# Optimization experiments

Measured on AMD Instinct MI355X. Metric: run time of the kernel, lower is better.

Reference implementation:

```python
import jax, jax.numpy as jnp
import numpy as np

N, E, D, NHID, NOUT, G = 50000, 800000, 128, 512, 768, 512
EPS = 1e-5

def setup_inputs() -> dict:
    key = jax.random.key(0)
    ks = jax.random.split(key, 20)
    rn = lambda k, s: jax.random.normal(k, s, jnp.float32) * 0.05
    inp = {
        'x': jax.random.normal(ks[0], (N, D), jnp.float32),
        'edge_index': jax.random.randint(ks[1], (2, E), 0, N, jnp.int32),
        'batch': jnp.sort(jax.random.randint(ks[2], (N,), 0, G, jnp.int32)),
        # GCN convs 1..3 (weights stored [in, out])
        'W1': rn(ks[3], (D, D)), 'b1': jnp.zeros((D,), jnp.float32),
        'W2': rn(ks[4], (D, D)), 'b2': jnp.zeros((D,), jnp.float32),
        'W3': rn(ks[5], (D, D)), 'b3': jnp.zeros((D,), jnp.float32),
        # GAT attention layer (1 head)
        'Wa': rn(ks[6], (D, D)), 'ba': jnp.zeros((D,), jnp.float32),
        'a_src': rn(ks[7], (D,)), 'a_dst': rn(ks[8], (D,)),
        # BatchNorms: bn1, bn2, bn3, bn_attention stacked [4, D]
        'bn_gamma': jnp.ones((4, D), jnp.float32),
        'bn_beta': jnp.zeros((4, D), jnp.float32),
        # MLP head
        'Wm1': rn(ks[9], (D, NHID)), 'bm1': jnp.zeros((NHID,), jnp.float32),
        'Wm2': rn(ks[10], (NHID, NHID)), 'bm2': jnp.zeros((NHID,), jnp.float32),
        'Wm3': rn(ks[11], (NHID, NHID)), 'bm3': jnp.zeros((NHID,), jnp.float32),
        'Wm4': rn(ks[12], (NHID, NOUT)), 'bm4': jnp.zeros((NOUT,), jnp.float32),
    }
    return inp

def _bn(h, g, b):
    # BatchNorm1d over nodes, training-mode batch stats (biased variance)
    m = jnp.mean(h, axis=0)
    v = jnp.var(h, axis=0)
    return (h - m) * jax.lax.rsqrt(v + EPS) * g + b

def _gcn(x, W, b, src, dst, deg_isqrt):
    h = x @ W                               # [N, D]
    norm = deg_isqrt[src] * deg_isqrt[dst]  # [E+N]
    msg = h[src] * norm[:, None]            # gather + scale
    return jax.ops.segment_sum(msg, dst, num_segments=N) + b

def _gat(x, W, b, a_src, a_dst, src, dst):
    h = x @ W
    e = jax.nn.leaky_relu((h @ a_src)[src] + (h @ a_dst)[dst], 0.2)  # [E+N]
    m = jax.ops.segment_max(e, dst, num_segments=N)
    ex = jnp.exp(e - m[dst])
    den = jax.ops.segment_sum(ex, dst, num_segments=N)
    alpha = ex / den[dst]
    out = jax.ops.segment_sum(alpha[:, None] * h[src], dst, num_segments=N)
    return out + b

def reference(x, edge_index, batch, W1, b1, W2, b2, W3, b3, Wa, ba, a_src, a_dst,
              bn_gamma, bn_beta, Wm1, bm1, Wm2, bm2, Wm3, bm3, Wm4, bm4):
    # add self-loops (PyG GCNConv / GATConv default)
    loops = jnp.arange(N, dtype=edge_index.dtype)
    src = jnp.concatenate([edge_index[0], loops])
    dst = jnp.concatenate([edge_index[1], loops])
    deg = jax.ops.segment_sum(jnp.ones_like(dst, jnp.float32), dst, num_segments=N)
    deg_isqrt = jax.lax.rsqrt(deg)  # deg >= 1 thanks to self-loops

    relu = jax.nn.relu
    x = relu(_bn(_gcn(x, W1, b1, src, dst, deg_isqrt), bn_gamma[0], bn_beta[0])) + x
    x = relu(_bn(_gcn(x, W2, b2, src, dst, deg_isqrt), bn_gamma[1], bn_beta[1])) + x
    x = relu(_bn(_gcn(x, W3, b3, src, dst, deg_isqrt), bn_gamma[2], bn_beta[2])) + x
    x = relu(_bn(_gat(x, Wa, ba, a_src, a_dst, src, dst), bn_gamma[3], bn_beta[3])) + x

    # global mean pool over graphs
    counts = jax.ops.segment_sum(jnp.ones((N,), jnp.float32), batch, num_segments=G)
    pooled = jax.ops.segment_sum(x, batch, num_segments=G) / jnp.maximum(counts, 1.0)[:, None]

    h = relu(pooled @ Wm1 + bm1)
    h = relu(h @ Wm2 + bm2)
    h = relu(h @ Wm3 + bm3)
    return h @ Wm4 + bm4
```

## Files before the change

kernel.cpp:

```cpp
#include <hip/hip_runtime.h>
#include <stdint.h>

#define Nn   50000
#define Ee   800000
#define Dd   128
#define Gg   512
#define NHIDc 512
#define NOUTc 768
#define EPSf 1e-5f
#define CAP  64
#define PRNG 6250
#define NBPART 12500
#define NB2    250

#define OFF_CNT    0ul
#define OFF_ES     200192ul
#define OFF_ED     400384ul
#define OFF_STATS  600576ul
#define OFF_POOLED 601600ul
#define OFF_M1     863744ul
#define OFF_M2     1912320ul
#define OFF_COL    2960896ul
#define OFF_H      15760896ul
#define OFF_AGG    28560896ul
#define OFF_XCUR   41360896ul
#define OFF_PART   54160896ul
#define OFF_XBF    66960896ul

#define BF_LO(u) __uint_as_float((u) << 16)
#define BF_HI(u) __uint_as_float((u) & 0xffff0000u)

typedef __attribute__((ext_vector_type(8))) short bf16x8;
typedef __attribute__((ext_vector_type(4))) float f32x4;

__device__ inline uint32_t bfpack(float x, float y) {
    uint32_t ux = __float_as_uint(x), uy = __float_as_uint(y);
    ux += 0x7fff + ((ux >> 16) & 1);
    uy += 0x7fff + ((uy >> 16) & 1);
    return (ux >> 16) | (uy & 0xffff0000u);
}
__device__ inline short bf1(float x) {
    uint32_t u = __float_as_uint(x);
    u += 0x7fff + ((u >> 16) & 1);
    return (short)(u >> 16);
}
__device__ inline float wred16(float v) {
    v += __shfl_xor(v, 1); v += __shfl_xor(v, 2);
    v += __shfl_xor(v, 4); v += __shfl_xor(v, 8);
    return v;
}

__global__ void k_x2bf(const float* __restrict__ x, uint32_t* __restrict__ xbf) {
    int i = blockIdx.x * 256 + threadIdx.x;
    if (i < Nn * 16) {
        float4 a = reinterpret_cast<const float4*>(x)[2 * i];
        float4 b = reinterpret_cast<const float4*>(x)[2 * i + 1];
        uint32_t o[4] = {bfpack(a.x, a.y), bfpack(a.z, a.w),
                         bfpack(b.x, b.y), bfpack(b.z, b.w)};
        reinterpret_cast<uint4*>(xbf)[i] = *reinterpret_cast<uint4*>(o);
    }
}

__global__ void k_fill_init(int* cnt, int* colx) {
    int i = blockIdx.x * 256 + threadIdx.x;
    if (i < Nn) {
        cnt[i] = 1;
        colx[(size_t)i * CAP] = i;
    }
}

__global__ void k_bucket_fill(const int* __restrict__ ei, int* cnt, int* colx) {
    int grp = blockIdx.x & 7;
    int e = (blockIdx.x >> 3) * 256 + threadIdx.x;
    if (e >= Ee) return;
    int d = ei[Ee + e];
    if (d / PRNG != grp) return;
    int s = ei[e];
    int pos = atomicAdd(&cnt[d], 1);
    if (pos < CAP) colx[(size_t)d * CAP + pos] = s;
}

#define WTP 136
__global__ __launch_bounds__(512) void k_gemm_fused(
        const uint32_t* __restrict__ XP, const uint32_t* __restrict__ AggP,
        const float* __restrict__ stats, const float* __restrict__ W,
        const int* __restrict__ cntP,
        uint32_t* __restrict__ Hout, uint32_t* __restrict__ XoutP,
        const float* __restrict__ a_src, const float* __restrict__ a_dst,
        float* __restrict__ esO, float* __restrict__ edO) {
    __shared__ short WT[128 * WTP];
    __shared__ short XT[8][16 * WTP];
    __shared__ float isqL[128];

    int t = threadIdx.x;
    for (int i = t; i < 128 * 128; i += 512) {
        int k = i >> 7, c = i & 127;
        WT[c * WTP + k] = bf1(W[i]);
    }
    __syncthreads();

    int wave = t >> 6, lane = t & 63;
    int arow = lane & 15, kg = lane >> 4;
    int c4 = (lane * 4) & 63;
    int prow = lane >> 4;
    float scv[8], shv[8];
    if (stats) {
        #pragma unroll
        for (int j = 0; j < 8; ++j) {
            scv[j] = stats[2 * c4 + j];
            shv[j] = stats[128 + 2 * c4 + j];
        }
    }
    float asr[8], adr[8];
    if (esO) {
        #pragma unroll
        for (int jj = 0; jj < 8; ++jj) {
            asr[jj] = a_src[(lane & 15) * 8 + jj];
            adr[jj] = a_dst[(lane & 15) * 8 + jj];
        }
    }

    for (int tile = blockIdx.x * 128; tile < Nn; tile += gridDim.x * 128) {
        int rbase = tile + wave * 16;
        if (lane < 16) {
            int rg = rbase + lane;
            isqL[wave * 16 + lane] = (cntP && rg < Nn) ? rsqrtf((float)cntP[rg]) : 1.f;
        }
        uint32_t* xtw = reinterpret_cast<uint32_t*>(XT[wave]);
        #pragma unroll
        for (int b = 0; b < 4; ++b) {
            int row = b * 4 + prow;
            int rg = rbase + row;
            uint32_t xv[4] = {0u, 0u, 0u, 0u};
            if (rg < Nn) {
                *reinterpret_cast<uint4*>(xv) =
                    *reinterpret_cast<const uint4*>(&XP[(size_t)rg * 64 + c4]);
                if (AggP) {
                    uint32_t av[4];
                    *reinterpret_cast<uint4*>(av) =
                        *reinterpret_cast<const uint4*>(&AggP[(size_t)rg * 64 + c4]);
                    #pragma unroll
                    for (int q = 0; q < 4; ++q) {
                        float n0 = fmaxf(BF_LO(av[q]) * scv[2 * q] + shv[2 * q], 0.f) + BF_LO(xv[q]);
                        float n1 = fmaxf(BF_HI(av[q]) * scv[2 * q + 1] + shv[2 * q + 1], 0.f) + BF_HI(xv[q]);
                        xv[q] = bfpack(n0, n1);
                    }
                    *reinterpret_cast<uint4*>(&XoutP[(size_t)rg * 64 + c4]) =
                        *reinterpret_cast<uint4*>(xv);
                }
            }
            *reinterpret_cast<uint4*>(&xtw[row * (WTP / 2) + c4]) = *reinterpret_cast<uint4*>(xv);
        }
        bf16x8 afr[4];
        #pragma unroll
        for (int kt = 0; kt < 4; ++kt)
            afr[kt] = *reinterpret_cast<bf16x8*>(&XT[wave][arow * WTP + kt * 32 + kg * 8]);
        float sR[4];
        #pragma unroll
        for (int rr = 0; rr < 4; ++rr) sR[rr] = isqL[wave * 16 + kg * 4 + rr];

        #pragma unroll
        for (int ct = 0; ct < 8; ++ct) {
            int c = ct * 16 + arow;
            f32x4 acc = {0.f, 0.f, 0.f, 0.f};
            #pragma unroll
            for (int kt = 0; kt < 4; ++kt) {
                bf16x8 b = *reinterpret_cast<bf16x8*>(&WT[c * WTP + kt * 32 + kg * 8]);
                acc = __builtin_amdgcn_mfma_f32_16x16x32_bf16(afr[kt], b, acc, 0, 0, 0);
            }
            #pragma unroll
            for (int rr = 0; rr < 4; ++rr)
                XT[wave][(kg * 4 + rr) * WTP + c] = bf1(acc[rr] * sR[rr]);
        }
        #pragma unroll
        for (int p = 0; p < 4; ++p) {
            int rsl = p * 4 + kg;
            int rg = rbase + rsl;
            if (rg < Nn) {
                int chunk = lane & 15;
                bf16x8 vv = *reinterpret_cast<bf16x8*>(&XT[wave][rsl * WTP + chunk * 8]);
                *reinterpret_cast<bf16x8*>(reinterpret_cast<short*>(Hout) + (size_t)rg * 128 + chunk * 8) = vv;
                if (esO) {
                    float dsum = 0.f, ddum = 0.f;
                    #pragma unroll
                    for (int jj = 0; jj < 8; ++jj) {
                        float hv = __uint_as_float(((uint32_t)(unsigned short)vv[jj]) << 16);
                        dsum += hv * asr[jj];
                        ddum += hv * adr[jj];
                    }
                    dsum = wred16(dsum); ddum = wred16(ddum);
                    if ((lane & 15) == 0) { esO[rg] = dsum; edO[rg] = ddum; }
                }
            }
        }
    }
}

__global__ __launch_bounds__(256) void k_gcn_agg(const uint32_t* __restrict__ H,
                                                 const int* __restrict__ cnt,
                                                 const int* __restrict__ colx,
                                                 uint32_t* __restrict__ aggP,
                                                 float* __restrict__ part) {
    int wave = threadIdx.x >> 6, lane = threadIdx.x & 63;
    int half = lane >> 5, fl = lane & 31;
    int nid = blockIdx.x * 4 + wave;
    const uint2* H2 = reinterpret_cast<const uint2*>(H);

    int degF = cnt[nid];
    int deg = degF > CAP ? CAP : degF;
    size_t cb = (size_t)nid * CAP;
    int m = (deg - half + 1) >> 1;
    float f0a = 0.f, f1a = 0.f, f2a = 0.f, f3a = 0.f;
    float f0b = 0.f, f1b = 0.f, f2b = 0.f, f3b = 0.f;
    float f0c = 0.f, f1c = 0.f, f2c = 0.f, f3c = 0.f;
    float f0d = 0.f, f1d = 0.f, f2d = 0.f, f3d = 0.f;
    int k = 0;
    for (; k + 3 < m; k += 4) {
        int s0 = colx[cb + half + 2 * k];
        int s1 = colx[cb + half + 2 * k + 2];
        int s2 = colx[cb + half + 2 * k + 4];
        int s3 = colx[cb + half + 2 * k + 6];
        uint2 u0 = H2[(size_t)s0 * 32 + fl];
        uint2 u1 = H2[(size_t)s1 * 32 + fl];
        uint2 u2 = H2[(size_t)s2 * 32 + fl];
        uint2 u3 = H2[(size_t)s3 * 32 + fl];
        f0a += BF_LO(u0.x); f1a += BF_HI(u0.x); f2a += BF_LO(u0.y); f3a += BF_HI(u0.y);
        f0b += BF_LO(u1.x); f1b += BF_HI(u1.x); f2b += BF_LO(u1.y); f3b += BF_HI(u1.y);
        f0c += BF_LO(u2.x); f1c += BF_HI(u2.x); f2c += BF_LO(u2.y); f3c += BF_HI(u2.y);
        f0d += BF_LO(u3.x); f1d += BF_HI(u3.x); f2d += BF_LO(u3.y); f3d += BF_HI(u3.y);
    }
    for (; k < m; ++k) {
        int s0 = colx[cb + half + 2 * k];
        uint2 u0 = H2[(size_t)s0 * 32 + fl];
        f0a += BF_LO(u0.x); f1a += BF_HI(u0.x); f2a += BF_LO(u0.y); f3a += BF_HI(u0.y);
    }
    float f0 = (f0a + f0b) + (f0c + f0d);
    float f1 = (f1a + f1b) + (f1c + f1d);
    float f2 = (f2a + f2b) + (f2c + f2d);
    float f3 = (f3a + f3b) + (f3c + f3d);
    f0 += __shfl_xor(f0, 32); f1 += __shfl_xor(f1, 32);
    f2 += __shfl_xor(f2, 32); f3 += __shfl_xor(f3, 32);

    float o0 = 0.f, o1 = 0.f, o2 = 0.f, o3 = 0.f;
    if (half == 0) {
        float wd = rsqrtf((float)degF);
        o0 = f0 * wd; o1 = f1 * wd; o2 = f2 * wd; o3 = f3 * wd;
        uint2 o;
        o.x = bfpack(o0, o1);
        o.y = bfpack(o2, o3);
        reinterpret_cast<uint2*>(aggP)[(size_t)nid * 32 + fl] = o;
    }
    __shared__ float SS[4][128];
    __shared__ float QQ[4][128];
    if (half == 0) {
        SS[wave][4 * fl + 0] = o0; QQ[wave][4 * fl + 0] = o0 * o0;
        SS[wave][4 * fl + 1] = o1; QQ[wave][4 * fl + 1] = o1 * o1;
        SS[wave][4 * fl + 2] = o2; QQ[wave][4 * fl + 2] = o2 * o2;
        SS[wave][4 * fl + 3] = o3; QQ[wave][4 * fl + 3] = o3 * o3;
    }
    __syncthreads();
    int t = threadIdx.x;
    if (t < 128) {
        part[blockIdx.x * 256 + t]       = (SS[0][t] + SS[1][t]) + (SS[2][t] + SS[3][t]);
        part[blockIdx.x * 256 + 128 + t] = (QQ[0][t] + QQ[1][t]) + (QQ[2][t] + QQ[3][t]);
    }
}

__global__ __launch_bounds__(256) void k_gat_agg(const uint32_t* __restrict__ H,
                                                 const int* __restrict__ cnt,
                                                 const int* __restrict__ colx,
                                                 const float* __restrict__ es,
                                                 const float* __restrict__ ed,
                                                 uint32_t* __restrict__ aggP,
                                                 float* __restrict__ part) {
    int wave = threadIdx.x >> 6, lane = threadIdx.x & 63;
    int half = lane >> 5, fl = lane & 31;
    int nid = blockIdx.x * 4 + wave;
    const uint2* H2 = reinterpret_cast<const uint2*>(H);

    int degF = cnt[nid];
    int deg = degF > CAP ? CAP : degF;
    size_t cb = (size_t)nid * CAP;
    float edd = ed[nid];
    int m = (deg - half + 1) >> 1;
    float f0a = 0.f, f1a = 0.f, f2a = 0.f, f3a = 0.f, dena = 0.f;
    float f0b = 0.f, f1b = 0.f, f2b = 0.f, f3b = 0.f, denb = 0.f;
    float f0c = 0.f, f1c = 0.f, f2c = 0.f, f3c = 0.f, denc = 0.f;
    float f0d = 0.f, f1d = 0.f, f2d = 0.f, f3d = 0.f, dend = 0.f;
    int k = 0;
    for (; k + 3 < m; k += 4) {
        int s0 = colx[cb + half + 2 * k];
        int s1 = colx[cb + half + 2 * k + 2];
        int s2 = colx[cb + half + 2 * k + 4];
        int s3 = colx[cb + half + 2 * k + 6];
        float e0 = es[s0] + edd, e1 = es[s1] + edd;
        float e2 = es[s2] + edd, e3 = es[s3] + edd;
        e0 = (e0 < 0.f) ? 0.2f * e0 : e0;
        e1 = (e1 < 0.f) ? 0.2f * e1 : e1;
        e2 = (e2 < 0.f) ? 0.2f * e2 : e2;
        e3 = (e3 < 0.f) ? 0.2f * e3 : e3;
        float w0 = __expf(e0), w1 = __expf(e1), w2 = __expf(e2), w3 = __expf(e3);
        uint2 u0 = H2[(size_t)s0 * 32 + fl];
        uint2 u1 = H2[(size_t)s1 * 32 + fl];
        uint2 u2 = H2[(size_t)s2 * 32 + fl];
        uint2 u3 = H2[(size_t)s3 * 32 + fl];
        f0a += w0 * BF_LO(u0.x); f1a += w0 * BF_HI(u0.x);
        f2a += w0 * BF_LO(u0.y); f3a += w0 * BF_HI(u0.y); dena += w0;
        f0b += w1 * BF_LO(u1.x); f1b += w1 * BF_HI(u1.x);
        f2b += w1 * BF_LO(u1.y); f3b += w1 * BF_HI(u1.y); denb += w1;
        f0c += w2 * BF_LO(u2.x); f1c += w2 * BF_HI(u2.x);
        f2c += w2 * BF_LO(u2.y); f3c += w2 * BF_HI(u2.y); denc += w2;
        f0d += w3 * BF_LO(u3.x); f1d += w3 * BF_HI(u3.x);
        f2d += w3 * BF_LO(u3.y); f3d += w3 * BF_HI(u3.y); dend += w3;
    }
    for (; k < m; ++k) {
        int s0 = colx[cb + half + 2 * k];
        float e0 = es[s0] + edd;
        e0 = (e0 < 0.f) ? 0.2f * e0 : e0;
        float w0 = __expf(e0);
        uint2 u0 = H2[(size_t)s0 * 32 + fl];
        f0a += w0 * BF_LO(u0.x); f1a += w0 * BF_HI(u0.x);
        f2a += w0 * BF_LO(u0.y); f3a += w0 * BF_HI(u0.y); dena += w0;
    }
    float f0 = (f0a + f0b) + (f0c + f0d);
    float f1 = (f1a + f1b) + (f1c + f1d);
    float f2 = (f2a + f2b) + (f2c + f2d);
    float f3 = (f3a + f3b) + (f3c + f3d);
    float den = (dena + denb) + (denc + dend);
    f0 += __shfl_xor(f0, 32); f1 += __shfl_xor(f1, 32);
    f2 += __shfl_xor(f2, 32); f3 += __shfl_xor(f3, 32);
    den += __shfl_xor(den, 32);

    float o0 = 0.f, o1 = 0.f, o2 = 0.f, o3 = 0.f;
    if (half == 0) {
        float inv = 1.f / den;
        o0 = f0 * inv; o1 = f1 * inv; o2 = f2 * inv; o3 = f3 * inv;
        uint2 o;
        o.x = bfpack(o0, o1);
        o.y = bfpack(o2, o3);
        reinterpret_cast<uint2*>(aggP)[(size_t)nid * 32 + fl] = o;
    }
    __shared__ float SS[4][128];
    __shared__ float QQ[4][128];
    if (half == 0) {
        SS[wave][4 * fl + 0] = o0; QQ[wave][4 * fl + 0] = o0 * o0;
        SS[wave][4 * fl + 1] = o1; QQ[wave][4 * fl + 1] = o1 * o1;
        SS[wave][4 * fl + 2] = o2; QQ[wave][4 * fl + 2] = o2 * o2;
        SS[wave][4 * fl + 3] = o3; QQ[wave][4 * fl + 3] = o3 * o3;
    }
    __syncthreads();
    int t = threadIdx.x;
    if (t < 128) {
        part[blockIdx.x * 256 + t]       = (SS[0][t] + SS[1][t]) + (SS[2][t] + SS[3][t]);
        part[blockIdx.x * 256 + 128 + t] = (QQ[0][t] + QQ[1][t]) + (QQ[2][t] + QQ[3][t]);
    }
}

__global__ __launch_bounds__(256) void k_bn_red1(const float* __restrict__ part,
                                                 float* __restrict__ part2) {
    int t = threadIdx.x;
    int r0 = blockIdx.x * 50;
    float acc = 0.f;
    #pragma unroll 5
    for (int r = r0; r < r0 + 50; ++r) acc += part[(size_t)r * 256 + t];
    part2[blockIdx.x * 256 + t] = acc;
}

__global__ __launch_bounds__(256) void k_bn_final(const float* __restrict__ part2, float* stats,
                                                  const float* __restrict__ gamma,
                                                  const float* __restrict__ beta) {
    int f = blockIdx.x;
    int t = threadIdx.x;
    float s = 0.f, q = 0.f;
    if (t < NB2) {
        s = part2[t * 256 + f];
        q = part2[t * 256 + 128 + f];
    }
    #pragma unroll
    for (int o = 32; o > 0; o >>= 1) { s += __shfl_xor(s, o); q += __shfl_xor(q, o); }
    __shared__ float rs[4], rq[4];
    if ((t & 63) == 0) { rs[t >> 6] = s; rq[t >> 6] = q; }
    __syncthreads();
    if (t == 0) {
        float S = (rs[0] + rs[1]) + (rs[2] + rs[3]);
        float Q = (rq[0] + rq[1]) + (rq[2] + rq[3]);
        const float invN = 1.f / (float)Nn;
        float mean = S * invN;
        float var = Q * invN - mean * mean;
        float scv = rsqrtf(var + EPSf) * gamma[f];
        stats[f] = scv;
        stats[128 + f] = beta[f] - mean * scv;
    }
}

__global__ __launch_bounds__(256) void k_pool(const uint32_t* __restrict__ AP,
                                              const float* __restrict__ stats,
                                              const uint32_t* __restrict__ XcP,
                                              const int* __restrict__ batch,
                                              float* __restrict__ pooled) {
    int g = blockIdx.x;
    int lo = 0, hi = Nn;
    while (lo < hi) { int mid = (lo + hi) >> 1; if (batch[mid] < g) lo = mid + 1; else hi = mid; }
    int start = lo;
    lo = start; hi = Nn;
    while (lo < hi) { int mid = (lo + hi) >> 1; if (batch[mid] < g + 1) lo = mid + 1; else hi = mid; }
    int end = lo;

    int f = threadIdx.x & 127, rg = threadIdx.x >> 7;
    float sc = stats[f], sh = stats[128 + f];
    float s = 0.f;
    for (int r = start + rg; r < end; r += 2) {
        uint32_t u = AP[(size_t)r * 64 + (f >> 1)];
        uint32_t ux = XcP[(size_t)r * 64 + (f >> 1)];
        float a  = (f & 1) ? BF_HI(u)  : BF_LO(u);
        float xv = (f & 1) ? BF_HI(ux) : BF_LO(ux);
        s += fmaxf(a * sc + sh, 0.f) + xv;
    }
    __shared__ float red[256];
    red[threadIdx.x] = s; __syncthreads();
    if (threadIdx.x < 128) {
        float tot = red[threadIdx.x] + red[threadIdx.x + 128];
        float cntg = (float)(end - start);
        pooled[g * Dd + threadIdx.x] = (cntg > 0.f) ? tot / cntg : 0.f;
    }
}

__global__ __launch_bounds__(256) void k_mlp32(const float* __restrict__ A,
                                               const float* __restrict__ B,
                                               const float* __restrict__ bias,
                                               float* __restrict__ C,
                                               int M, int K, int Nc, int do_relu) {
    __shared__ float Ast[64][36];
    __shared__ float Bs[64][68];

    int nbx = Nc >> 6;
    int by = blockIdx.x / nbx, bx = blockIdx.x - by * nbx;
    int r0 = by * 32, c0 = bx * 64;
    int t = threadIdx.x;
    int tc = t & 31, tr = t >> 5;

    float2 acc0 = {0, 0}, acc1 = {0, 0}, acc2 = {0, 0}, acc3 = {0, 0};

    int sar = t >> 3, sak = (t & 7) * 8;
    int sbk = t >> 2, sbc = (t & 3) * 16;

    for (int kc = 0; kc < K; kc += 64) {
        {
            const float* ap = A + (size_t)(r0 + sar) * K + kc + sak;
            float4 v0 = *reinterpret_cast<const float4*>(ap);
            float4 v1 = *reinterpret_cast<const float4*>(ap + 4);
            Ast[sak + 0][sar] = v0.x; Ast[sak + 1][sar] = v0.y;
            Ast[sak + 2][sar] = v0.z; Ast[sak + 3][sar] = v0.w;
            Ast[sak + 4][sar] = v1.x; Ast[sak + 5][sar] = v1.y;
            Ast[sak + 6][sar] = v1.z; Ast[sak + 7][sar] = v1.w;
        }
        {
            const float* bp = B + (size_t)(kc + sbk) * Nc + c0 + sbc;
            float4 w0 = *reinterpret_cast<const float4*>(bp);
            float4 w1 = *reinterpret_cast<const float4*>(bp + 4);
            float4 w2 = *reinterpret_cast<const float4*>(bp + 8);
            float4 w3 = *reinterpret_cast<const float4*>(bp + 12);
            *reinterpret_cast<float4*>(&Bs[sbk][sbc]) = w0;
            *reinterpret_cast<float4*>(&Bs[sbk][sbc + 4]) = w1;
            *reinterpret_cast<float4*>(&Bs[sbk][sbc + 8]) = w2;
            *reinterpret_cast<float4*>(&Bs[sbk][sbc + 12]) = w3;
        }
        __syncthreads();
        #pragma unroll 8
        for (int k = 0; k < 64; ++k) {
            float4 a = *reinterpret_cast<float4*>(&Ast[k][tr * 4]);
            float2 b = *reinterpret_cast<float2*>(&Bs[k][tc * 2]);
            acc0.x += a.x * b.x; acc0.y += a.x * b.y;
            acc1.x += a.y * b.x; acc1.y += a.y * b.y;
            acc2.x += a.z * b.x; acc2.y += a.z * b.y;
            acc3.x += a.w * b.x; acc3.y += a.w * b.y;
        }
        __syncthreads();
    }

    float b0 = bias[c0 + tc * 2], b1 = bias[c0 + tc * 2 + 1];
    float2 r[4] = {{acc0.x + b0, acc0.y + b1}, {acc1.x + b0, acc1.y + b1},
                   {acc2.x + b0, acc2.y + b1}, {acc3.x + b0, acc3.y + b1}};
    if (do_relu) {
        #pragma unroll
        for (int i = 0; i < 4; ++i) {
            r[i].x = fmaxf(r[i].x, 0.f); r[i].y = fmaxf(r[i].y, 0.f);
        }
    }
    #pragma unroll
    for (int i = 0; i < 4; ++i)
        *reinterpret_cast<float2*>(C + (size_t)(r0 + tr * 4 + i) * Nc + c0 + tc * 2) = r[i];
}

extern "C" void kernel_launch(void* const* d_in, const int* in_sizes, int n_in,
                              void* d_out, int out_size, void* d_ws, size_t ws_size,
                              hipStream_t stream) {
    const float* x       = (const float*)d_in[0];
    const int*   ei      = (const int*)d_in[1];
    const int*   batch   = (const int*)d_in[2];
    const float* W1      = (const float*)d_in[3];
    const float* W2      = (const float*)d_in[5];
    const float* W3      = (const float*)d_in[7];
    const float* Wa      = (const float*)d_in[9];
    const float* a_src   = (const float*)d_in[11];
    const float* a_dst   = (const float*)d_in[12];
    const float* bn_g    = (const float*)d_in[13];
    const float* bn_b    = (const float*)d_in[14];
    const float* Wm1     = (const float*)d_in[15];
    const float* bm1     = (const float*)d_in[16];
    const float* Wm2     = (const float*)d_in[17];
    const float* bm2     = (const float*)d_in[18];
    const float* Wm3     = (const float*)d_in[19];
    const float* bm3     = (const float*)d_in[20];
    const float* Wm4     = (const float*)d_in[21];
    const float* bm4     = (const float*)d_in[22];

    char* ws = (char*)d_ws;
    int*      cnt    = (int*)(ws + OFF_CNT);
    float*    es     = (float*)(ws + OFF_ES);
    float*    ed     = (float*)(ws + OFF_ED);
    float*    stats  = (float*)(ws + OFF_STATS);
    float*    pooled = (float*)(ws + OFF_POOLED);
    float*    m1     = (float*)(ws + OFF_M1);
    float*    m2     = (float*)(ws + OFF_M2);
    int*      colx   = (int*)(ws + OFF_COL);
    uint32_t* h      = (uint32_t*)(ws + OFF_H);
    uint32_t* aggP   = (uint32_t*)(ws + OFF_AGG);
    uint32_t* xcurP  = (uint32_t*)(ws + OFF_XCUR);
    float*    part   = (float*)(ws + OFF_PART);
    uint32_t* xbf    = (uint32_t*)(ws + OFF_XBF);
    float*    part2  = m1;

    const int nb196 = 196;
    const int nbE8  = ((Ee + 255) / 256) * 8;
    const int nbGemm = (Nn + 127) / 128;
    const int nbX2  = (Nn * 16 + 255) / 256;

    k_x2bf<<<nbX2, 256, 0, stream>>>(x, xbf);
    k_fill_init<<<nb196, 256, 0, stream>>>(cnt, colx);
    k_bucket_fill<<<nbE8, 256, 0, stream>>>(ei, cnt, colx);

    k_gemm_fused<<<nbGemm, 512, 0, stream>>>(xbf, nullptr, nullptr, W1, cnt, h, nullptr,
                                             nullptr, nullptr, nullptr, nullptr);
    k_gcn_agg<<<NBPART, 256, 0, stream>>>(h, cnt, colx, aggP, part);
    k_bn_red1<<<NB2, 256, 0, stream>>>(part, part2);
    k_bn_final<<<128, 256, 0, stream>>>(part2, stats, bn_g + 0 * Dd, bn_b + 0 * Dd);

    k_gemm_fused<<<nbGemm, 512, 0, stream>>>(xbf, aggP, stats, W2, cnt, h, xcurP,
                                             nullptr, nullptr, nullptr, nullptr);
    k_gcn_agg<<<NBPART, 256, 0, stream>>>(h, cnt, colx, aggP, part);
    k_bn_red1<<<NB2, 256, 0, stream>>>(part, part2);
    k_bn_final<<<128, 256, 0, stream>>>(part2, stats, bn_g + 1 * Dd, bn_b + 1 * Dd);

    k_gemm_fused<<<nbGemm, 512, 0, stream>>>(xcurP, aggP, stats, W3, cnt, h, xcurP,
                                             nullptr, nullptr, nullptr, nullptr);
    k_gcn_agg<<<NBPART, 256, 0, stream>>>(h, cnt, colx, aggP, part);
    k_bn_red1<<<NB2, 256, 0, stream>>>(part, part2);
    k_bn_final<<<128, 256, 0, stream>>>(part2, stats, bn_g + 2 * Dd, bn_b + 2 * Dd);

    k_gemm_fused<<<nbGemm, 512, 0, stream>>>(xcurP, aggP, stats, Wa, nullptr, h, xcurP,
                                             a_src, a_dst, es, ed);
    k_gat_agg<<<NBPART, 256, 0, stream>>>(h, cnt, colx, es, ed, aggP, part);
    k_bn_red1<<<NB2, 256, 0, stream>>>(part, part2);
    k_bn_final<<<128, 256, 0, stream>>>(part2, stats, bn_g + 3 * Dd, bn_b + 3 * Dd);

    k_pool<<<Gg, 256, 0, stream>>>(aggP, stats, xcurP, batch, pooled);

    k_mlp32<<<(Gg / 32) * (NHIDc / 64), 256, 0, stream>>>(pooled, Wm1, bm1, m1, Gg, Dd, NHIDc, 1);
    k_mlp32<<<(Gg / 32) * (NHIDc / 64), 256, 0, stream>>>(m1, Wm2, bm2, m2, Gg, NHIDc, NHIDc, 1);
    k_mlp32<<<(Gg / 32) * (NHIDc / 64), 256, 0, stream>>>(m2, Wm3, bm3, m1, Gg, NHIDc, NHIDc, 1);
    k_mlp32<<<(Gg / 32) * (NOUTc / 64), 256, 0, stream>>>(m1, Wm4, bm4, (float*)d_out, Gg, NHIDc, NOUTc, 0);
}
```

Baseline: 372.4 us.

## Merge prep kernels, fuse BN reductions with ticket, use bf16 MFMA for MLP head

Three changes. The bf16 conversion and bucket-init kernels are merged into one prep kernel. The two-stage BatchNorm statistics reduction becomes a single kernel using float atomics and a last-block ticket. The fp32 SIMT MLP head GEMMs are replaced with bf16 MFMA 16x16x32 tiles of 64x64. Together these remove several launches and speed up the small GEMMs, at the cost of bf16 rounding in the MLP and nondeterministic atomic summation order. One hazard: statsAcc and the ticket alias the m2 buffer, which the MLP head later overwrites, but the BN launches all come before that.

Measured after the change: 406.4 us. 9.1% more time.

```diff
diff --git a/kernel.cpp b/kernel.cpp
--- a/kernel.cpp
+++ b/kernel.cpp
@@ -11,7 +11,7 @@
 #define CAP  64
 #define PRNG 6250
 #define NBPART 12500
-#define NB2    250
+#define NBRED  250
 
 #define OFF_CNT    0ul
 #define OFF_ES     200192ul
@@ -50,23 +50,22 @@
     return v;
 }
 
-__global__ void k_x2bf(const float* __restrict__ x, uint32_t* __restrict__ xbf) {
+__global__ void k_prep(const float* __restrict__ x, uint32_t* __restrict__ xbf,
+                       int* cnt, int* colx, float* statsAcc, int* ticket) {
     int i = blockIdx.x * 256 + threadIdx.x;
-    if (i < Nn * 16) {
+    {
         float4 a = reinterpret_cast<const float4*>(x)[2 * i];
         float4 b = reinterpret_cast<const float4*>(x)[2 * i + 1];
         uint32_t o[4] = {bfpack(a.x, a.y), bfpack(a.z, a.w),
                          bfpack(b.x, b.y), bfpack(b.z, b.w)};
         reinterpret_cast<uint4*>(xbf)[i] = *reinterpret_cast<uint4*>(o);
     }
-}
-
-__global__ void k_fill_init(int* cnt, int* colx) {
-    int i = blockIdx.x * 256 + threadIdx.x;
     if (i < Nn) {
         cnt[i] = 1;
         colx[(size_t)i * CAP] = i;
     }
+    if (i < 256) statsAcc[i] = 0.f;
+    if (i == 256) *ticket = 0;
 }
 
 __global__ void k_bucket_fill(const int* __restrict__ ei, int* cnt, int* colx) {
@@ -356,40 +355,39 @@
     }
 }
 
-__global__ __launch_bounds__(256) void k_bn_red1(const float* __restrict__ part,
-                                                 float* __restrict__ part2) {
+__global__ __launch_bounds__(256) void k_bn_redfin(const float* __restrict__ part,
+                                                   float* statsAcc, int* ticket,
+                                                   float* stats,
+                                                   const float* __restrict__ gamma,
+                                                   const float* __restrict__ beta) {
     int t = threadIdx.x;
     int r0 = blockIdx.x * 50;
     float acc = 0.f;
     #pragma unroll 5
     for (int r = r0; r < r0 + 50; ++r) acc += part[(size_t)r * 256 + t];
-    part2[blockIdx.x * 256 + t] = acc;
-}
-
-__global__ __launch_bounds__(256) void k_bn_final(const float* __restrict__ part2, float* stats,
-                                                  const float* __restrict__ gamma,
-                                                  const float* __restrict__ beta) {
-    int f = blockIdx.x;
-    int t = threadIdx.x;
-    float s = 0.f, q = 0.f;
-    if (t < NB2) {
-        s = part2[t * 256 + f];
-        q = part2[t * 256 + 128 + f];
-    }
-    #pragma unroll
-    for (int o = 32; o > 0; o >>= 1) { s += __shfl_xor(s, o); q += __shfl_xor(q, o); }
-    __shared__ float rs[4], rq[4];
-    if ((t & 63) == 0) { rs[t >> 6] = s; rq[t >> 6] = q; }
+    atomicAdd(&statsAcc[t], acc);
+    __threadfence();
     __syncthreads();
-    if (t == 0) {
-        float S = (rs[0] + rs[1]) + (rs[2] + rs[3]);
-        float Q = (rq[0] + rq[1]) + (rq[2] + rq[3]);
-        const float invN = 1.f / (float)Nn;
-        float mean = S * invN;
-        float var = Q * invN - mean * mean;
-        float scv = rsqrtf(var + EPSf) * gamma[f];
-        stats[f] = scv;
-        stats[128 + f] = beta[f] - mean * scv;
+    __shared__ int amLast;
+    if (t == 0) amLast = (atomicAdd(ticket, 1) == NBRED - 1) ? 1 : 0;
+    __syncthreads();
+    if (amLast) {
+        float S = 0.f, Q = 0.f;
+        if (t < 128) {
+            S = atomicAdd(&statsAcc[t], 0.f);
+            Q = atomicAdd(&statsAcc[128 + t], 0.f);
+        }
+        __syncthreads();
+        atomicExch(&statsAcc[t], 0.f);
+        if (t == 0) atomicExch(ticket, 0);
+        if (t < 128) {
+            const float invN = 1.f / (float)Nn;
+            float mean = S * invN;
+            float var = Q * invN - mean * mean;
+            float scv = rsqrtf(var + EPSf) * gamma[t];
+            stats[t] = scv;
+            stats[128 + t] = beta[t] - mean * scv;
+        }
     }
 }
 
@@ -425,71 +423,94 @@
     }
 }
 
-__global__ __launch_bounds__(256) void k_mlp32(const float* __restrict__ A,
-                                               const float* __restrict__ B,
-                                               const float* __restrict__ bias,
-                                               float* __restrict__ C,
-                                               int M, int K, int Nc, int do_relu) {
-    __shared__ float Ast[64][36];
-    __shared__ float Bs[64][68];
+#define ASTR 80
+__global__ __launch_bounds__(256) void k_mlp_mfma(const float* __restrict__ A,
+                                                  const float* __restrict__ B,
+                                                  const float* __restrict__ bias,
+                                                  float* __restrict__ C,
+                                                  int M, int K, int Nc, int do_relu) {
+    __shared__ short As[64 * ASTR];
+    __shared__ short Bs[64 * ASTR];
 
     int nbx = Nc >> 6;
     int by = blockIdx.x / nbx, bx = blockIdx.x - by * nbx;
-    int r0 = by * 32, c0 = bx * 64;
+    int r0 = by * 64, n0 = bx * 64;
     int t = threadIdx.x;
-    int tc = t & 31, tr = t >> 5;
-
-    float2 acc0 = {0, 0}, acc1 = {0, 0}, acc2 = {0, 0}, acc3 = {0, 0};
-
-    int sar = t >> 3, sak = (t & 7) * 8;
-    int sbk = t >> 2, sbc = (t & 3) * 16;
+    int wave = t >> 6, lane = t & 63;
+    int arow = lane & 15, kg = lane >> 4;
+    int sr = t >> 2, sc = (t & 3) * 16;
+
+    f32x4 acc0 = {0, 0, 0, 0}, acc1 = {0, 0, 0, 0};
+    f32x4 acc2 = {0, 0, 0, 0}, acc3 = {0, 0, 0, 0};
 
     for (int kc = 0; kc < K; kc += 64) {
         {
-            const float* ap = A + (size_t)(r0 + sar) * K + kc + sak;
+            const float* ap = A + (size_t)(r0 + sr) * K + kc + sc;
             float4 v0 = *reinterpret_cast<const float4*>(ap);
             float4 v1 = *reinterpret_cast<const float4*>(ap + 4);
-            Ast[sak + 0][sar] = v0.x; Ast[sak + 1][sar] = v0.y;
-            Ast[sak + 2][sar] = v0.z; Ast[sak + 3][sar] = v0.w;
-            Ast[sak + 4][sar] = v1.x; Ast[sak + 5][sar] = v1.y;
-            Ast[sak + 6][sar] = v1.z; Ast[sak + 7][sar] = v1.w;
+            float4 v2 = *reinterpret_cast<const float4*>(ap + 8);
+            float4 v3 = *reinterpret_cast<const float4*>(ap + 12);
+            uint32_t o[8] = {bfpack(v0.x, v0.y), bfpack(v0.z, v0.w),
+                             bfpack(v1.x, v1.y), bfpack(v1.z, v1.w),
+                             bfpack(v2.x, v2.y), bfpack(v2.z, v2.w),
+                             bfpack(v3.x, v3.y), bfpack(v3.z, v3.w)};
+            *reinterpret_cast<uint4*>(&As[sr * ASTR + sc])     = *reinterpret_cast<uint4*>(&o[0]);
+            *reinterpret_cast<uint4*>(&As[sr * ASTR + sc + 8]) = *reinterpret_cast<uint4*>(&o[4]);
         }
         {
-            const float* bp = B + (size_t)(kc + sbk) * Nc + c0 + sbc;
+            const float* bp = B + (size_t)(kc + sr) * Nc + n0 + sc;
             float4 w0 = *reinterpret_cast<const float4*>(bp);
             float4 w1 = *reinterpret_cast<const float4*>(bp + 4);
             float4 w2 = *reinterpret_cast<const float4*>(bp + 8);
             float4 w3 = *reinterpret_cast<const float4*>(bp + 12);
-            *reinterpret_cast<float4*>(&Bs[sbk][sbc]) = w0;
-            *reinterpret_cast<float4*>(&Bs[sbk][sbc + 4]) = w1;
-            *reinterpret_cast<float4*>(&Bs[sbk][sbc + 8]) = w2;
-            *reinterpret_cast<float4*>(&Bs[sbk][sbc + 12]) = w3;
+            float wv[16] = {w0.x, w0.y, w0.z, w0.w, w1.x, w1.y, w1.z, w1.w,
+                            w2.x, w2.y, w2.z, w2.w, w3.x, w3.y, w3.z, w3.w};
+            #pragma unroll
+            for (int j = 0; j < 16; ++j)
+                Bs[(sc + j) * ASTR + sr] = bf1(wv[j]);
         }
         __syncthreads();
-        #pragma unroll 8
-        for (int k = 0; k < 64; ++k) {
-            float4 a = *reinterpret_cast<float4*>(&Ast[k][tr * 4]);
-            float2 b = *reinterpret_cast<float2*>(&Bs[k][tc * 2]);
-            acc0.x += a.x * b.x; acc0.y += a.x * b.y;
-            acc1.x += a.y * b.x; acc1.y += a.y * b.y;
-            acc2.x += a.z * b.x; acc2.y += a.z * b.y;
-            acc3.x += a.w * b.x; acc3.y += a.w * b.y;
+        bf16x8 a0 = *reinterpret_cast<bf16x8*>(&As[(wave * 16 + arow) * ASTR + kg * 8]);
+        bf16x8 a1 = *reinterpret_cast<bf16x8*>(&As[(wave * 16 + arow) * ASTR + 32 + kg * 8]);
+        {
+            bf16x8 b0 = *reinterpret_cast<bf16x8*>(&Bs[(0 * 16 + arow) * ASTR + kg * 8]);
+            bf16x8 b1 = *reinterpret_cast<bf16x8*>(&Bs[(0 * 16 + arow) * ASTR + 32 + kg * 8]);
+            acc0 = __builtin_amdgcn_mfma_f32_16x16x32_bf16(a0, b0, acc0, 0, 0, 0);
+            acc0 = __builtin_amdgcn_mfma_f32_16x16x32_bf16(a1, b1, acc0, 0, 0, 0);
+        }
+        {
+            bf16x8 b0 = *reinterpret_cast<bf16x8*>(&Bs[(1 * 16 + arow) * ASTR + kg * 8]);
+            bf16x8 b1 = *reinterpret_cast<bf16x8*>(&Bs[(1 * 16 + arow) * ASTR + 32 + kg * 8]);
+            acc1 = __builtin_amdgcn_mfma_f32_16x16x32_bf16(a0, b0, acc1, 0, 0, 0);
+            acc1 = __builtin_amdgcn_mfma_f32_16x16x32_bf16(a1, b1, acc1, 0, 0, 0);
+        }
+        {
+            bf16x8 b0 = *reinterpret_cast<bf16x8*>(&Bs[(2 * 16 + arow) * ASTR + kg * 8]);
+            bf16x8 b1 = *reinterpret_cast<bf16x8*>(&Bs[(2 * 16 + arow) * ASTR + 32 + kg * 8]);
+            acc2 = __builtin_amdgcn_mfma_f32_16x16x32_bf16(a0, b0, acc2, 0, 0, 0);
+            acc2 = __builtin_amdgcn_mfma_f32_16x16x32_bf16(a1, b1, acc2, 0, 0, 0);
+        }
+        {
+            bf16x8 b0 = *reinterpret_cast<bf16x8*>(&Bs[(3 * 16 + arow) * ASTR + kg * 8]);
+            bf16x8 b1 = *reinterpret_cast<bf16x8*>(&Bs[(3 * 16 + arow) * ASTR + 32 + kg * 8]);
+            acc3 = __builtin_amdgcn_mfma_f32_16x16x32_bf16(a0, b0, acc3, 0, 0, 0);
+            acc3 = __builtin_amdgcn_mfma_f32_16x16x32_bf16(a1, b1, acc3, 0, 0, 0);
         }
         __syncthreads();
     }
-
-    float b0 = bias[c0 + tc * 2], b1 = bias[c0 + tc * 2 + 1];
-    float2 r[4] = {{acc0.x + b0, acc0.y + b1}, {acc1.x + b0, acc1.y + b1},
-                   {acc2.x + b0, acc2.y + b1}, {acc3.x + b0, acc3.y + b1}};
-    if (do_relu) {
-        #pragma unroll
-        for (int i = 0; i < 4; ++i) {
-            r[i].x = fmaxf(r[i].x, 0.f); r[i].y = fmaxf(r[i].y, 0.f);
-        }
-    }
     #pragma unroll
-    for (int i = 0; i < 4; ++i)
-        *reinterpret_cast<float2*>(C + (size_t)(r0 + tr * 4 + i) * Nc + c0 + tc * 2) = r[i];
+    for (int ct = 0; ct < 4; ++ct) {
+        f32x4 acc = (ct == 0) ? acc0 : (ct == 1) ? acc1 : (ct == 2) ? acc2 : acc3;
+        int col = n0 + ct * 16 + arow;
+        float bv = bias[col];
+        #pragma unroll
+        for (int rr = 0; rr < 4; ++rr) {
+            int row = r0 + wave * 16 + kg * 4 + rr;
+            float v = acc[rr] + bv;
+            if (do_relu) v = fmaxf(v, 0.f);
+            C[(size_t)row * Nc + col] = v;
+        }
+    }
 }
 
 extern "C" void kernel_launch(void* const* d_in, const int* in_sizes, int n_in,
@@ -529,45 +550,40 @@
     uint32_t* xcurP  = (uint32_t*)(ws + OFF_XCUR);
     float*    part   = (float*)(ws + OFF_PART);
     uint32_t* xbf    = (uint32_t*)(ws + OFF_XBF);
-    float*    part2  = m1;
-
-    const int nb196 = 196;
+    float*    statsAcc = m2;
+    int*      ticket   = (int*)(m2 + 256);
+
     const int nbE8  = ((Ee + 255) / 256) * 8;
     const int nbGemm = (Nn + 127) / 128;
-    const int nbX2  = (Nn * 16 + 255) / 256;
-
-    k_x2bf<<<nbX2, 256, 0, stream>>>(x, xbf);
-    k_fill_init<<<nb196, 256, 0, stream>>>(cnt, colx);
+    const int nbPrep = (Nn * 16 + 255) / 256;
+
+    k_prep<<<nbPrep, 256, 0, stream>>>(x, xbf, cnt, colx, statsAcc, ticket);
     k_bucket_fill<<<nbE8, 256, 0, stream>>>(ei, cnt, colx);
 
     k_gemm_fused<<<nbGemm, 512, 0, stream>>>(xbf, nullptr, nullptr, W1, cnt, h, nullptr,
                                              nullptr, nullptr, nullptr, nullptr);
     k_gcn_agg<<<NBPART, 256, 0, stream>>>(h, cnt, colx, aggP, part);
-    k_bn_red1<<<NB2, 256, 0, stream>>>(part, part2);
-    k_bn_final<<<128, 256, 0, stream>>>(part2, stats, bn_g + 0 * Dd, bn_b + 0 * Dd);
+    k_bn_redfin<<<NBRED, 256, 0, stream>>>(part, statsAcc, ticket, stats, bn_g + 0 * Dd, bn_b + 0 * Dd);
 
     k_gemm_fused<<<nbGemm, 512, 0, stream>>>(xbf, aggP, stats, W2, cnt, h, xcurP,
                                              nullptr, nullptr, nullptr, nullptr);
     k_gcn_agg<<<NBPART, 256, 0, stream>>>(h, cnt, colx, aggP, part);
-    k_bn_red1<<<NB2, 256, 0, stream>>>(part, part2);
-    k_bn_final<<<128, 256, 0, stream>>>(part2, stats, bn_g + 1 * Dd, bn_b + 1 * Dd);
+    k_bn_redfin<<<NBRED, 256, 0, stream>>>(part, statsAcc, ticket, stats, bn_g + 1 * Dd, bn_b + 1 * Dd);
 
     k_gemm_fused<<<nbGemm, 512, 0, stream>>>(xcurP, aggP, stats, W3, cnt, h, xcurP,
                                              nullptr, nullptr, nullptr, nullptr);
     k_gcn_agg<<<NBPART, 256, 0, stream>>>(h, cnt, colx, aggP, part);
-    k_bn_red1<<<NB2, 256, 0, stream>>>(part, part2);
-    k_bn_final<<<128, 256, 0, stream>>>(part2, stats, bn_g + 2 * Dd, bn_b + 2 * Dd);
+    k_bn_redfin<<<NBRED, 256, 0, stream>>>(part, statsAcc, ticket, stats, bn_g + 2 * Dd, bn_b + 2 * Dd);
 
     k_gemm_fused<<<nbGemm, 512, 0, stream>>>(xcurP, aggP, stats, Wa, nullptr, h, xcurP,
                                              a_src, a_dst, es, ed);
     k_gat_agg<<<NBPART, 256, 0, stream>>>(h, cnt, colx, es, ed, aggP, part);
-    k_bn_red1<<<NB2, 256, 0, stream>>>(part, part2);
-    k_bn_final<<<128, 256, 0, stream>>>(part2, stats, bn_g + 3 * Dd, bn_b + 3 * Dd);
+    k_bn_redfin<<<NBRED, 256, 0, stream>>>(part, statsAcc, ticket, stats, bn_g + 3 * Dd, bn_b + 3 * Dd);
 
     k_pool<<<Gg, 256, 0, stream>>>(aggP, stats, xcurP, batch, pooled);
 
-    k_mlp32<<<(Gg / 32) * (NHIDc / 64), 256, 0, stream>>>(pooled, Wm1, bm1, m1, Gg, Dd, NHIDc, 1);
-    k_mlp32<<<(Gg / 32) * (NHIDc / 64), 256, 0, stream>>>(m1, Wm2, bm2, m2, Gg, NHIDc, NHIDc, 1);
-    k_mlp32<<<(Gg / 32) * (NHIDc / 64), 256, 0, stream>>>(m2, Wm3, bm3, m1, Gg, NHIDc, NHIDc, 1);
-    k_mlp32<<<(Gg / 32) * (NOUTc / 64), 256, 0, stream>>>(m1, Wm4, bm4, (float*)d_out, Gg, NHIDc, NOUTc, 0);
-}
+    k_mlp_mfma<<<(Gg / 64) * (NHIDc / 64), 256, 0, stream>>>(pooled, Wm1, bm1, m1, Gg, Dd, NHIDc, 1);
+    k_mlp_mfma<<<(Gg / 64) * (NHIDc / 64), 256, 0, stream>>>(m1, Wm2, bm2, m2, Gg, NHIDc, NHIDc, 1);
+    k_mlp_mfma<<<(Gg / 64) * (NHIDc / 64), 256, 0, stream>>>(m2, Wm3, bm3, m1, Gg, NHIDc, NHIDc, 1);
+    k_mlp_mfma<<<(Gg / 64) * (NOUTc / 64), 256, 0, stream>>>(m1, Wm4, bm4, (float*)d_out, Gg, NHIDc, NOUTc, 0);
+}
```
